# Performance work log

Hardware: AMD Instinct MI355X
Metric: run time of the kernel (lower is better)

The kernel has to match this reference:

```python
import jax, jax.numpy as jnp
import numpy as np

B, S, D, H = 4, 2048, 1024, 16
DEPTH = D // H  # 64


def setup_inputs() -> dict:
    key = jax.random.key(0)
    ks = jax.random.split(key, 7)
    scale = 1.0 / np.sqrt(D)
    return {
        "x": jax.random.normal(ks[0], (B, S, D), dtype=jnp.float32),
        "y": jax.random.normal(ks[1], (B, S, D), dtype=jnp.float32),
        "bias": jax.random.normal(ks[2], (1, 1, S, S), dtype=jnp.float32),
        "Wq": jax.random.normal(ks[3], (D, D), dtype=jnp.float32) * scale,
        "Wk": jax.random.normal(ks[4], (D, D), dtype=jnp.float32) * scale,
        "Wv": jax.random.normal(ks[5], (D, D), dtype=jnp.float32) * scale,
        "Wo": jax.random.normal(ks[6], (D, D), dtype=jnp.float32) * scale,
    }


def _split_heads(t):
    # [B, S, D] -> [B, H, S, depth]
    b, s, _ = t.shape
    return t.reshape(b, s, H, DEPTH).transpose(0, 2, 1, 3)


def reference(x, y, bias, Wq, Wk, Wv, Wo):
    # nn.Linear(bias=False): out = in @ W.T
    q = _split_heads(x @ Wq.T) * (DEPTH ** -0.5)  # [B,H,Sx,depth]
    k = _split_heads(y @ Wk.T)                    # [B,H,Sy,depth]
    v = _split_heads(y @ Wv.T)                    # [B,H,Sy,depth]
    logits = jnp.einsum('bhqd,bhkd->bhqk', q, k) + bias  # [B,H,Sx,Sy]
    weights = jax.nn.softmax(logits, axis=-1)
    attn = jnp.einsum('bhqk,bhkd->bhqd', weights, v)     # [B,H,Sx,depth]
    # combine heads: [B,H,Sx,depth] -> [B,Sx,D]
    attn = attn.transpose(0, 2, 1, 3).reshape(x.shape[0], x.shape[1], D)
    return attn @ Wo.T
```

## Files before the change

kernel.cpp:

```cpp
#include <hip/hip_runtime.h>
#include <hip/hip_bf16.h>

#define Bn 4
#define Sn 2048
#define Dn 1024
#define Hn 16
#define DEPTHn 64

typedef __attribute__((ext_vector_type(8))) short short8;
typedef __attribute__((ext_vector_type(4))) float float4v;

#define LOG2E 1.44269504088896340736f
#define C16   23.083120654223414f

__device__ __forceinline__ void load_lds16(const void* g, void* l) {
  __builtin_amdgcn_global_load_lds(
      (const __attribute__((address_space(1))) unsigned int*)g,
      (__attribute__((address_space(3))) unsigned int*)l, 16, 0, 0);
}

__global__ __launch_bounds__(256) void cast_bf16(const float* __restrict__ in,
                                                 __hip_bfloat16* __restrict__ out,
                                                 int n8, float scale) {
  int i = blockIdx.x * blockDim.x + threadIdx.x;
  if (i >= n8) return;
  float v[8];
  *(float4*)&v[0] = ((const float4*)in)[2 * i];
  *(float4*)&v[4] = ((const float4*)in)[2 * i + 1];
  union { __hip_bfloat16 h[8]; short8 s; } u;
#pragma unroll
  for (int k = 0; k < 8; ++k) u.h[k] = __float2bfloat16(v[k] * scale);
  ((short8*)out)[i] = u.s;
}

__global__ __launch_bounds__(256) void cast_w(const float* __restrict__ wq,
                                              const float* __restrict__ wk,
                                              const float* __restrict__ wv,
                                              const float* __restrict__ wo,
                                              __hip_bfloat16* __restrict__ out) {
  int i = blockIdx.x * blockDim.x + threadIdx.x;
  int which = i >> 17, j = i & 131071;
  const float* src = (which == 0) ? wq : (which == 1) ? wk : (which == 2) ? wv : wo;
  float scale = (which == 0) ? 0.125f : 1.0f;
  float v[8];
  *(float4*)&v[0] = ((const float4*)src)[2 * j];
  *(float4*)&v[4] = ((const float4*)src)[2 * j + 1];
  union { __hip_bfloat16 h[8]; short8 s; } u;
#pragma unroll
  for (int k = 0; k < 8; ++k) u.h[k] = __float2bfloat16(v[k] * scale);
  ((short8*)out)[i] = u.s;
}

__global__ __launch_bounds__(256) void rearrange_bias(const float* __restrict__ in,
                                                      float* __restrict__ out) {
  int t = blockIdx.x * blockDim.x + threadIdx.x;
  int r = t & 3, lane = (t >> 2) & 63, wm = (t >> 8) & 15;
  int jti = (t >> 12) & 15, qb = (t >> 16) & 7;
  int wave = wm >> 2, mt = wm & 3, quad = lane >> 4, l16 = lane & 15;
  int row = qb * 256 + wave * 64 + mt * 16 + quad * 4 + r;
  const float* src = in + (size_t)row * Sn + jti * 128 + l16;
  float4v o0, o1;
#pragma unroll
  for (int j = 0; j < 4; ++j) o0[j] = fmaf(src[j * 16], LOG2E, -C16);
#pragma unroll
  for (int j = 0; j < 4; ++j) o1[j] = fmaf(src[(j + 4) * 16], LOG2E, -C16);
  ((float4v*)out)[t * 2] = o0;
  ((float4v*)out)[t * 2 + 1] = o1;
}

template <int MODE>
__global__ __launch_bounds__(256) void gemm_bt(const __hip_bfloat16* __restrict__ A,
                                               const __hip_bfloat16* __restrict__ B,
                                               float* __restrict__ Cf,
                                               __hip_bfloat16* __restrict__ Cb1,
                                               __hip_bfloat16* __restrict__ Cb2) {
  constexpr int Kdim = 1024;
  __shared__ __hip_bfloat16 As[128 * 64];
  __shared__ __hip_bfloat16 Bs[128 * 64];
  const int tid = threadIdx.x;
  const int wave = tid >> 6, lane = tid & 63;
  const int quad = lane >> 4, l16 = lane & 15;
  const int bm = blockIdx.x, bn = blockIdx.y;
  const int wm = (wave & 1) * 64, wn = (wave >> 1) * 64;

  const __hip_bfloat16* aptr[4];
  const __hip_bfloat16* bptr[4];
#pragma unroll
  for (int i = 0; i < 4; ++i) {
    int c = wave * 4 + i;
    aptr[i] = A + (size_t)(bm * 128 + c * 8 + (lane >> 3)) * Kdim + (lane & 7) * 8;
    bptr[i] = B + (size_t)(bn * 128 + c * 8 + (lane >> 3)) * Kdim + (lane & 7) * 8;
  }

  float4v acc[4][4];
#pragma unroll
  for (int i = 0; i < 4; ++i)
#pragma unroll
    for (int j = 0; j < 4; ++j) acc[i][j] = (float4v){0.f, 0.f, 0.f, 0.f};

  for (int kt = 0; kt < Kdim / 64; ++kt) {
    __syncthreads();
#pragma unroll
    for (int i = 0; i < 4; ++i) {
      int c = wave * 4 + i;
      load_lds16(aptr[i] + kt * 64, &As[c * 512]);
      load_lds16(bptr[i] + kt * 64, &Bs[c * 512]);
    }
    __syncthreads();
#pragma unroll
    for (int ks = 0; ks < 2; ++ks) {
      short8 af[4], bf[4];
#pragma unroll
      for (int i = 0; i < 4; ++i)
        af[i] = *(const short8*)&As[(wm + i * 16 + l16) * 64 + ks * 32 + quad * 8];
#pragma unroll
      for (int j = 0; j < 4; ++j)
        bf[j] = *(const short8*)&Bs[(wn + j * 16 + l16) * 64 + ks * 32 + quad * 8];
#pragma unroll
      for (int i = 0; i < 4; ++i)
#pragma unroll
        for (int j = 0; j < 4; ++j)
          acc[i][j] = __builtin_amdgcn_mfma_f32_16x16x32_bf16(af[i], bf[j], acc[i][j], 0, 0, 0);
    }
  }

#pragma unroll
  for (int i = 0; i < 4; ++i)
#pragma unroll
    for (int j = 0; j < 4; ++j)
#pragma unroll
      for (int r = 0; r < 4; ++r) {
        int row = bm * 128 + wm + i * 16 + quad * 4 + r;
        int col = bn * 128 + wn + j * 16 + l16;
        float v = acc[i][j][r];
        int b = row >> 11, s = row & 2047;
        if (MODE == 2) {
          Cf[(size_t)row * 1024 + col] = v;
        } else if (MODE == 0) {
          int h = col >> 6, d = col & 63;
          int d2 = d ^ ((s & 7) << 3);
          Cb1[(((size_t)b * Hn + h) * Sn + s) * DEPTHn + d2] = __float2bfloat16(v);
        } else {
          if (col < 1024) {
            int h = col >> 6, d = col & 63;
            int d2 = d ^ ((s & 7) << 3);
            Cb1[(((size_t)b * Hn + h) * Sn + s) * DEPTHn + d2] = __float2bfloat16(v);
          } else {
            int n = col - 1024;
            int h = n >> 6, d = n & 63;
            int jl = s & 127;
            int sig = ((jl & 15) << 3) | (jl >> 4);
            int inner = sig ^ ((d & 7) << 3);
            int s2 = (s & ~127) | inner;
            Cb2[(((size_t)b * Hn + h) * DEPTHn + d) * Sn + s2] = __float2bfloat16(v);
          }
        }
      }
}

__global__ __launch_bounds__(256, 2) void flash_attn(const __hip_bfloat16* __restrict__ Q,
                                                     const __hip_bfloat16* __restrict__ Kh,
                                                     const __hip_bfloat16* __restrict__ Vt,
                                                     const float* __restrict__ biasR,
                                                     __hip_bfloat16* __restrict__ O) {
  __shared__ __hip_bfloat16 Ks[128 * 64];
  __shared__ __hip_bfloat16 Vts[64 * 128];
  __shared__ __hip_bfloat16 Ps[4][32 * 128];
  const int tid = threadIdx.x;
  const int wave = tid >> 6, lane = tid & 63;
  const int quad = lane >> 4, l16 = lane & 15;
  const int swk = (l16 & 7) << 3;
  const int bh = blockIdx.y, qb = blockIdx.x;
  const int q0 = qb * 256;
  const __hip_bfloat16* Qp = Q + (size_t)bh * Sn * DEPTHn;
  const __hip_bfloat16* Kp = Kh + (size_t)bh * Sn * DEPTHn;
  const __hip_bfloat16* Vp = Vt + (size_t)bh * DEPTHn * Sn;

  short8 qf[4][2];
#pragma unroll
  for (int mt = 0; mt < 4; ++mt)
#pragma unroll
    for (int ks = 0; ks < 2; ++ks)
      qf[mt][ks] = *(const short8*)&Qp[(size_t)(q0 + wave * 64 + mt * 16 + l16) * 64 +
                                       ((ks * 32 + quad * 8) ^ swk)];

  float l_i[4][4];
  float4v oacc[4][4];
#pragma unroll
  for (int mt = 0; mt < 4; ++mt)
#pragma unroll
    for (int r = 0; r < 4; ++r) l_i[mt][r] = 0.f;
#pragma unroll
  for (int mt = 0; mt < 4; ++mt)
#pragma unroll
    for (int nt = 0; nt < 4; ++nt) oacc[mt][nt] = (float4v){0.f, 0.f, 0.f, 0.f};

  const int koff = (lane >> 3) * 64 + (lane & 7) * 8;
  const int voff = (lane >> 4) * Sn + l16 * 8;

  for (int jti = 0; jti < 16; ++jti) {
    const int j0 = jti * 128;
    __syncthreads();
#pragma unroll
    for (int i = 0; i < 4; ++i) {
      int c = wave * 4 + i;
      load_lds16(Kp + (size_t)(j0 + c * 8) * 64 + koff, &Ks[c * 512]);
      load_lds16(Vp + (size_t)(c * 4) * Sn + j0 + voff, &Vts[c * 512]);
    }
    __syncthreads();

#pragma unroll
    for (int mtp = 0; mtp < 2; ++mtp) {
      float4v sacc[2][8];
#pragma unroll
      for (int m2 = 0; m2 < 2; ++m2)
#pragma unroll
        for (int jt = 0; jt < 8; ++jt) sacc[m2][jt] = (float4v){0.f, 0.f, 0.f, 0.f};
#pragma unroll
      for (int ks = 0; ks < 2; ++ks) {
        short8 kf[8];
#pragma unroll
        for (int jt = 0; jt < 8; ++jt)
          kf[jt] = *(const short8*)&Ks[(jt * 16 + l16) * 64 + ((ks * 32 + quad * 8) ^ swk)];
#pragma unroll
        for (int m2 = 0; m2 < 2; ++m2)
#pragma unroll
          for (int jt = 0; jt < 8; ++jt)
            sacc[m2][jt] = __builtin_amdgcn_mfma_f32_16x16x32_bf16(qf[mtp * 2 + m2][ks], kf[jt],
                                                                   sacc[m2][jt], 0, 0, 0);
      }

#pragma unroll
      for (int m2 = 0; m2 < 2; ++m2) {
        const int mt = mtp * 2 + m2;
        const float4v* bp = (const float4v*)biasR +
                            ((((size_t)(qb * 16 + jti) * 16 + wave * 4 + mt) * 64 + lane) << 3);
#pragma unroll
        for (int r = 0; r < 4; ++r) {
          float4v b0 = bp[r * 2], b1 = bp[r * 2 + 1];
          float ls = 0.f;
          union { __hip_bfloat16 h[8]; short8 s8; } pu;
#pragma unroll
          for (int jt = 0; jt < 8; ++jt) {
            float bb = (jt < 4) ? b0[jt] : b1[jt - 4];
            float p = __builtin_amdgcn_exp2f(fmaf(sacc[m2][jt][r], LOG2E, bb));
            ls += p;
            pu.h[jt] = __float2bfloat16(p);
          }
          l_i[mt][r] += ls;
          const int prow = m2 * 16 + quad * 4 + r;
          *(short8*)&Ps[wave][prow * 128 + ((l16 ^ (prow & 7)) << 3)] = pu.s8;
        }
      }

#pragma unroll
      for (int ks = 0; ks < 4; ++ks) {
        short8 vf[4];
#pragma unroll
        for (int nt = 0; nt < 4; ++nt)
          vf[nt] = *(const short8*)&Vts[(nt * 16 + l16) * 128 + ((ks * 32 + quad * 8) ^ swk)];
#pragma unroll
        for (int m2 = 0; m2 < 2; ++m2) {
          short8 pf = *(const short8*)&Ps[wave][(m2 * 16 + l16) * 128 +
                                               ((ks * 32 + quad * 8) ^ swk)];
#pragma unroll
          for (int nt = 0; nt < 4; ++nt)
            oacc[mtp * 2 + m2][nt] =
                __builtin_amdgcn_mfma_f32_16x16x32_bf16(pf, vf[nt], oacc[mtp * 2 + m2][nt], 0, 0, 0);
        }
      }
    }
  }

  const int b = bh >> 4, h = bh & 15;
#pragma unroll
  for (int mt = 0; mt < 4; ++mt) {
    float inv[4];
#pragma unroll
    for (int r = 0; r < 4; ++r) {
      float l = l_i[mt][r];
#pragma unroll
      for (int off = 1; off < 16; off <<= 1) l += __shfl_xor(l, off, 64);
      inv[r] = __builtin_amdgcn_rcpf(l);
    }
#pragma unroll
    for (int nt = 0; nt < 4; ++nt)
#pragma unroll
      for (int r = 0; r < 4; ++r) {
        int s = q0 + wave * 64 + mt * 16 + quad * 4 + r;
        int d = nt * 16 + l16;
        O[((size_t)b * Sn + s) * Dn + h * 64 + d] = __float2bfloat16(oacc[mt][nt][r] * inv[r]);
      }
  }
}

extern "C" void kernel_launch(void* const* d_in, const int* in_sizes, int n_in,
                              void* d_out, int out_size, void* d_ws, size_t ws_size,
                              hipStream_t stream) {
  const float* x = (const float*)d_in[0];
  const float* y = (const float*)d_in[1];
  const float* bias = (const float*)d_in[2];
  const float* Wq = (const float*)d_in[3];
  const float* Wk = (const float*)d_in[4];
  const float* Wv = (const float*)d_in[5];
  const float* Wo = (const float*)d_in[6];
  float* out = (float*)d_out;

  const size_t SZ_XY = (size_t)Bn * Sn * Dn * 2;
  const size_t SZ_W = (size_t)Dn * Dn * 2;
  const size_t SZ_BIASF = (size_t)Sn * Sn * 4;

  char* p = (char*)d_ws;
  __hip_bfloat16* xb = (__hip_bfloat16*)p;      p += SZ_XY;
  __hip_bfloat16* yb = (__hip_bfloat16*)p;      p += SZ_XY;
  __hip_bfloat16* wqb = (__hip_bfloat16*)p;     p += SZ_W;
  __hip_bfloat16* wkb = (__hip_bfloat16*)p;     p += SZ_W;
  __hip_bfloat16* wvb = (__hip_bfloat16*)p;     p += SZ_W;
  __hip_bfloat16* wob = (__hip_bfloat16*)p;     p += SZ_W;
  float* biasR = (float*)p;                     p += SZ_BIASF;
  __hip_bfloat16* Qb = (__hip_bfloat16*)p;      p += SZ_XY;
  __hip_bfloat16* Kb = (__hip_bfloat16*)p;      p += SZ_XY;
  __hip_bfloat16* Vtb = (__hip_bfloat16*)p;     p += SZ_XY;
  __hip_bfloat16* attnb = (__hip_bfloat16*)p;   p += SZ_XY;

  const int nXY8 = Bn * Sn * Dn / 8;

  cast_bf16<<<nXY8 / 256, 256, 0, stream>>>(x, xb, nXY8, 1.0f);
  cast_bf16<<<nXY8 / 256, 256, 0, stream>>>(y, yb, nXY8, 1.0f);
  cast_w<<<(4 * Dn * Dn / 8) / 256, 256, 0, stream>>>(Wq, Wk, Wv, Wo, wqb);
  rearrange_bias<<<(Sn * Sn / 8) / 256, 256, 0, stream>>>(bias, biasR);

  gemm_bt<0><<<dim3(64, 8), 256, 0, stream>>>(xb, wqb, nullptr, Qb, nullptr);
  gemm_bt<3><<<dim3(64, 16), 256, 0, stream>>>(yb, wkb, nullptr, Kb, Vtb);

  flash_attn<<<dim3(8, 64), 256, 0, stream>>>(Qb, Kb, Vtb, biasR, attnb);

  gemm_bt<2><<<dim3(64, 8), 256, 0, stream>>>(attnb, wob, out, nullptr, nullptr);
}
```

Before: 444.7 us.

## Fuse QKV projections into one GEMM with LDS-transposed V store and swizzled attention grid

Merges the x and y casts into one launch and the Q and KV projection GEMMs into a single 64x24 grid kernel that selects its input by column block. V-tile outputs are staged through padded LDS so the transposed Vt layout is written as contiguous 16-byte chunks, replacing the scattered per-element strided stores. The flash attention grid is linearized and remapped so consecutive blocks span different batch-heads. The aim is fewer launches, better wave fill and coalesced V writes; the V path adds LDS traffic and extra syncs, and the Vt swizzle layout changes, which must match the attention kernel's reads.

```diff
diff --git a/kernel.cpp b/kernel.cpp
--- a/kernel.cpp
+++ b/kernel.cpp
@@ -19,17 +19,18 @@
       (__attribute__((address_space(3))) unsigned int*)l, 16, 0, 0);
 }
 
-__global__ __launch_bounds__(256) void cast_bf16(const float* __restrict__ in,
-                                                 __hip_bfloat16* __restrict__ out,
-                                                 int n8, float scale) {
+__global__ __launch_bounds__(256) void cast_xy(const float* __restrict__ x,
+                                               const float* __restrict__ y,
+                                               __hip_bfloat16* __restrict__ out) {
   int i = blockIdx.x * blockDim.x + threadIdx.x;
-  if (i >= n8) return;
+  const float* src = (i >> 20) ? y : x;
+  int j = i & 1048575;
   float v[8];
-  *(float4*)&v[0] = ((const float4*)in)[2 * i];
-  *(float4*)&v[4] = ((const float4*)in)[2 * i + 1];
+  *(float4*)&v[0] = ((const float4*)src)[2 * j];
+  *(float4*)&v[4] = ((const float4*)src)[2 * j + 1];
   union { __hip_bfloat16 h[8]; short8 s; } u;
 #pragma unroll
-  for (int k = 0; k < 8; ++k) u.h[k] = __float2bfloat16(v[k] * scale);
+  for (int k = 0; k < 8; ++k) u.h[k] = __float2bfloat16(v[k]);
   ((short8*)out)[i] = u.s;
 }
 
@@ -68,12 +69,114 @@
   ((float4v*)out)[t * 2 + 1] = o1;
 }
 
-template <int MODE>
-__global__ __launch_bounds__(256) void gemm_bt(const __hip_bfloat16* __restrict__ A,
-                                               const __hip_bfloat16* __restrict__ B,
-                                               float* __restrict__ Cf,
-                                               __hip_bfloat16* __restrict__ Cb1,
-                                               __hip_bfloat16* __restrict__ Cb2) {
+__global__ __launch_bounds__(256) void gemm_qkv(const __hip_bfloat16* __restrict__ Xb,
+                                                const __hip_bfloat16* __restrict__ Yb,
+                                                const __hip_bfloat16* __restrict__ Wqkv,
+                                                __hip_bfloat16* __restrict__ Qb,
+                                                __hip_bfloat16* __restrict__ Kb,
+                                                __hip_bfloat16* __restrict__ Vtb) {
+  constexpr int Kdim = 1024;
+  __shared__ char pool[128 * 129 * 2];
+  __hip_bfloat16* As = (__hip_bfloat16*)pool;
+  __hip_bfloat16* Bs = As + 128 * 64;
+  __hip_bfloat16* Sg = (__hip_bfloat16*)pool;
+
+  const int tid = threadIdx.x;
+  const int wave = tid >> 6, lane = tid & 63;
+  const int quad = lane >> 4, l16 = lane & 15;
+  const int bm = blockIdx.x, bn = blockIdx.y;
+  const int sel = bn >> 3;
+  const int wm = (wave & 1) * 64, wn = (wave >> 1) * 64;
+  const __hip_bfloat16* A = (sel == 0) ? Xb : Yb;
+
+  const __hip_bfloat16* aptr[4];
+  const __hip_bfloat16* bptr[4];
+#pragma unroll
+  for (int i = 0; i < 4; ++i) {
+    int c = wave * 4 + i;
+    aptr[i] = A + (size_t)(bm * 128 + c * 8 + (lane >> 3)) * Kdim + (lane & 7) * 8;
+    bptr[i] = Wqkv + (size_t)(bn * 128 + c * 8 + (lane >> 3)) * Kdim + (lane & 7) * 8;
+  }
+
+  float4v acc[4][4];
+#pragma unroll
+  for (int i = 0; i < 4; ++i)
+#pragma unroll
+    for (int j = 0; j < 4; ++j) acc[i][j] = (float4v){0.f, 0.f, 0.f, 0.f};
+
+  for (int kt = 0; kt < Kdim / 64; ++kt) {
+    __syncthreads();
+#pragma unroll
+    for (int i = 0; i < 4; ++i) {
+      int c = wave * 4 + i;
+      load_lds16(aptr[i] + kt * 64, &As[c * 512]);
+      load_lds16(bptr[i] + kt * 64, &Bs[c * 512]);
+    }
+    __syncthreads();
+#pragma unroll
+    for (int ks = 0; ks < 2; ++ks) {
+      short8 af[4], bf[4];
+#pragma unroll
+      for (int i = 0; i < 4; ++i)
+        af[i] = *(const short8*)&As[(wm + i * 16 + l16) * 64 + ks * 32 + quad * 8];
+#pragma unroll
+      for (int j = 0; j < 4; ++j)
+        bf[j] = *(const short8*)&Bs[(wn + j * 16 + l16) * 64 + ks * 32 + quad * 8];
+#pragma unroll
+      for (int i = 0; i < 4; ++i)
+#pragma unroll
+        for (int j = 0; j < 4; ++j)
+          acc[i][j] = __builtin_amdgcn_mfma_f32_16x16x32_bf16(af[i], bf[j], acc[i][j], 0, 0, 0);
+    }
+  }
+
+  const int b = bm >> 4;
+  if (sel < 2) {
+    __hip_bfloat16* dst = (sel == 0) ? Qb : Kb;
+    const int nbase = (bn & 7) * 128;
+#pragma unroll
+    for (int i = 0; i < 4; ++i)
+#pragma unroll
+      for (int j = 0; j < 4; ++j)
+#pragma unroll
+        for (int r = 0; r < 4; ++r) {
+          int row = bm * 128 + wm + i * 16 + quad * 4 + r;
+          int col = nbase + wn + j * 16 + l16;
+          int s = row & 2047, h = col >> 6, d = col & 63;
+          int d2 = d ^ ((s & 7) << 3);
+          dst[(((size_t)b * Hn + h) * Sn + s) * DEPTHn + d2] = __float2bfloat16(acc[i][j][r]);
+        }
+  } else {
+    __syncthreads();
+#pragma unroll
+    for (int i = 0; i < 4; ++i)
+#pragma unroll
+      for (int j = 0; j < 4; ++j)
+#pragma unroll
+        for (int r = 0; r < 4; ++r) {
+          int row = wm + i * 16 + quad * 4 + r;
+          int col = wn + j * 16 + l16;
+          Sg[row * 129 + col] = __float2bfloat16(acc[i][j][r]);
+        }
+    __syncthreads();
+    const int s_tile = (bm & 15) * 128;
+#pragma unroll
+    for (int iter = 0; iter < 8; ++iter) {
+      int id = iter * 256 + tid;
+      int chunk = id & 15, lcol = id >> 4;
+      int hg = (bn - 16) * 2 + (lcol >> 6), d = lcol & 63;
+      int c = chunk ^ (d & 7);
+      union { __hip_bfloat16 h[8]; short8 s8; } pu;
+#pragma unroll
+      for (int i = 0; i < 8; ++i) pu.h[i] = Sg[(i * 16 + c) * 129 + lcol];
+      *(short8*)&Vtb[(((size_t)b * Hn + hg) * DEPTHn + d) * Sn + s_tile + chunk * 8] = pu.s8;
+    }
+  }
+}
+
+__global__ __launch_bounds__(256) void gemm_out(const __hip_bfloat16* __restrict__ A,
+                                                const __hip_bfloat16* __restrict__ B,
+                                                float* __restrict__ Cf) {
   constexpr int Kdim = 1024;
   __shared__ __hip_bfloat16 As[128 * 64];
   __shared__ __hip_bfloat16 Bs[128 * 64];
@@ -123,7 +226,6 @@
           acc[i][j] = __builtin_amdgcn_mfma_f32_16x16x32_bf16(af[i], bf[j], acc[i][j], 0, 0, 0);
     }
   }
-
 #pragma unroll
   for (int i = 0; i < 4; ++i)
 #pragma unroll
@@ -132,29 +234,7 @@
       for (int r = 0; r < 4; ++r) {
         int row = bm * 128 + wm + i * 16 + quad * 4 + r;
         int col = bn * 128 + wn + j * 16 + l16;
-        float v = acc[i][j][r];
-        int b = row >> 11, s = row & 2047;
-        if (MODE == 2) {
-          Cf[(size_t)row * 1024 + col] = v;
-        } else if (MODE == 0) {
-          int h = col >> 6, d = col & 63;
-          int d2 = d ^ ((s & 7) << 3);
-          Cb1[(((size_t)b * Hn + h) * Sn + s) * DEPTHn + d2] = __float2bfloat16(v);
-        } else {
-          if (col < 1024) {
-            int h = col >> 6, d = col & 63;
-            int d2 = d ^ ((s & 7) << 3);
-            Cb1[(((size_t)b * Hn + h) * Sn + s) * DEPTHn + d2] = __float2bfloat16(v);
-          } else {
-            int n = col - 1024;
-            int h = n >> 6, d = n & 63;
-            int jl = s & 127;
-            int sig = ((jl & 15) << 3) | (jl >> 4);
-            int inner = sig ^ ((d & 7) << 3);
-            int s2 = (s & ~127) | inner;
-            Cb2[(((size_t)b * Hn + h) * DEPTHn + d) * Sn + s2] = __float2bfloat16(v);
-          }
-        }
+        Cf[(size_t)row * 1024 + col] = acc[i][j][r];
       }
 }
 
@@ -170,7 +250,9 @@
   const int wave = tid >> 6, lane = tid & 63;
   const int quad = lane >> 4, l16 = lane & 15;
   const int swk = (l16 & 7) << 3;
-  const int bh = blockIdx.y, qb = blockIdx.x;
+  const int lin = blockIdx.x;
+  const int bh = (lin & 7) * 8 + ((lin >> 3) & 7);
+  const int qb = lin >> 6;
   const int q0 = qb * 256;
   const __hip_bfloat16* Qp = Q + (size_t)bh * Sn * DEPTHn;
   const __hip_bfloat16* Kp = Kh + (size_t)bh * Sn * DEPTHn;
@@ -313,9 +395,7 @@
   char* p = (char*)d_ws;
   __hip_bfloat16* xb = (__hip_bfloat16*)p;      p += SZ_XY;
   __hip_bfloat16* yb = (__hip_bfloat16*)p;      p += SZ_XY;
-  __hip_bfloat16* wqb = (__hip_bfloat16*)p;     p += SZ_W;
-  __hip_bfloat16* wkb = (__hip_bfloat16*)p;     p += SZ_W;
-  __hip_bfloat16* wvb = (__hip_bfloat16*)p;     p += SZ_W;
+  __hip_bfloat16* wqkv = (__hip_bfloat16*)p;    p += 3 * SZ_W;
   __hip_bfloat16* wob = (__hip_bfloat16*)p;     p += SZ_W;
   float* biasR = (float*)p;                     p += SZ_BIASF;
   __hip_bfloat16* Qb = (__hip_bfloat16*)p;      p += SZ_XY;
@@ -323,17 +403,13 @@
   __hip_bfloat16* Vtb = (__hip_bfloat16*)p;     p += SZ_XY;
   __hip_bfloat16* attnb = (__hip_bfloat16*)p;   p += SZ_XY;
 
-  const int nXY8 = Bn * Sn * Dn / 8;
-
-  cast_bf16<<<nXY8 / 256, 256, 0, stream>>>(x, xb, nXY8, 1.0f);
-  cast_bf16<<<nXY8 / 256, 256, 0, stream>>>(y, yb, nXY8, 1.0f);
-  cast_w<<<(4 * Dn * Dn / 8) / 256, 256, 0, stream>>>(Wq, Wk, Wv, Wo, wqb);
+  cast_xy<<<2 * 1048576 / 256, 256, 0, stream>>>(x, y, xb);
+  cast_w<<<(4 * Dn * Dn / 8) / 256, 256, 0, stream>>>(Wq, Wk, Wv, Wo, wqkv);
   rearrange_bias<<<(Sn * Sn / 8) / 256, 256, 0, stream>>>(bias, biasR);
 
-  gemm_bt<0><<<dim3(64, 8), 256, 0, stream>>>(xb, wqb, nullptr, Qb, nullptr);
-  gemm_bt<3><<<dim3(64, 16), 256, 0, stream>>>(yb, wkb, nullptr, Kb, Vtb);
-
-  flash_attn<<<dim3(8, 64), 256, 0, stream>>>(Qb, Kb, Vtb, biasR, attnb);
-
-  gemm_bt<2><<<dim3(64, 8), 256, 0, stream>>>(attnb, wob, out, nullptr, nullptr);
-}
+  gemm_qkv<<<dim3(64, 24), 256, 0, stream>>>(xb, yb, wqkv, Qb, Kb, Vtb);
+
+  flash_attn<<<512, 256, 0, stream>>>(Qb, Kb, Vtb, biasR, attnb);
+
+  gemm_out<<<dim3(64, 8), 256, 0, stream>>>(attnb, wob, out);
+}
```

Result: faster. 392.8 us (-11.7%).
